# Kernel optimization log

Hardware: AMD Instinct MI355X
Metric: run time of the kernel (lower is better)

Reference implementation:

```python
import jax, jax.numpy as jnp
import numpy as np

# Dimensions (see shape_source)
IN_VEC = 131072          # input_vector_size
NUM_CAPS = 512           # num_capsules (output capsules)
CAP_SIZE = 256           # capsule_size
RF_SIZE = 64             # receptive_field_size
RF_PER_CAP = CAP_SIZE // RF_SIZE        # 4
IN_CAPS = IN_VEC // CAP_SIZE            # 512 input_eff_capsules
CONN_P = 0.1             # connection_probability


def setup_inputs() -> dict:
    key = jax.random.key(0)
    kx, kc, kw = jax.random.split(key, 3)
    x = jax.random.normal(kx, (IN_VEC,), dtype=jnp.float32)
    # Sparse ScRRAMBLe routing tensor: mostly zeros, gated by connection probability.
    # Shape (input_eff_capsules, rf_per_cap_in, num_capsules, rf_per_cap_out) per einsum 'ijkl,ijm->klm'.
    Ci = (jax.random.uniform(kc, (IN_CAPS, RF_PER_CAP, NUM_CAPS, RF_PER_CAP)) < CONN_P).astype(jnp.float32)
    # glorot_normal over last two axes: fan_in = fan_out = RF_SIZE -> std = sqrt(2/(64+64)) = 0.125
    glorot_std = float(np.sqrt(2.0 / (RF_SIZE + RF_SIZE)))
    Wi = glorot_std * jax.random.normal(kw, (NUM_CAPS, RF_PER_CAP, RF_PER_CAP, RF_SIZE, RF_SIZE), dtype=jnp.float32)
    return {"x": x, "Ci": Ci, "Wi": Wi}


def reference(x, Ci, Wi):
    # x: (IN_VEC,) -> (input_eff_capsules, rf_per_cap, rf_size)
    x_reshaped = x.reshape(IN_CAPS, RF_PER_CAP, RF_SIZE)
    # Route input receptive fields to output capsule slots:
    # x_routed: (num_capsules, rf_per_cap, rf_size)
    x_routed = jnp.einsum('ijkl,ijm->klm', Ci, x_reshaped)
    # Per-capsule small batched transform:
    # y: (num_capsules, rf_per_cap, rf_size)
    y = jnp.einsum('ijklm,ikm->ijl', Wi, x_routed)
    return y
```

## Files before the change

### kernel.cpp

```cpp
#include <hip/hip_runtime.h>


typedef float f4 __attribute__((ext_vector_type(4)));

#define NCH 8

__global__ __launch_bounds__(256) void route_kernel(
    const float* __restrict__ x,
    const float* __restrict__ Ci,
    float* __restrict__ xr_part)
{
    const int iq  = blockIdx.x;
    const int c   = blockIdx.y;
    const int t   = threadIdx.x;
    const int il  = t >> 6;
    const int g   = (t >> 4) & 3;
    const int mq4 = t & 15;
    const int i   = (iq << 2) + il;

    const f4* __restrict__ Ci4 = (const f4*)Ci;
    const f4* __restrict__ x4  = (const f4*)x;

    __shared__ f4 part[1024];

    f4 a0 = {0.f,0.f,0.f,0.f};
    f4 a1 = {0.f,0.f,0.f,0.f};
    f4 a2 = {0.f,0.f,0.f,0.f};
    f4 a3 = {0.f,0.f,0.f,0.f};

    const int ijpc = 2048 / NCH;
    const int sub  = ijpc >> 2;
    const int base = c * ijpc + g * sub;
    #pragma unroll 4
    for (int it = 0; it < sub; ++it) {
        const int ij = base + it;
        const f4 c4 = Ci4[ij * 512 + i];
        const f4 xv = x4[(ij << 4) + mq4];
        a0 += c4.x * xv;
        a1 += c4.y * xv;
        a2 += c4.z * xv;
        a3 += c4.w * xv;
    }

    const int pb = ((g << 2) + il) << 2;
    part[(pb + 0) * 16 + mq4] = a0;
    part[(pb + 1) * 16 + mq4] = a1;
    part[(pb + 2) * 16 + mq4] = a2;
    part[(pb + 3) * 16 + mq4] = a3;
    __syncthreads();

    const int il2 = t >> 6;
    const int r   = (t >> 4) & 3;
    const int mm  = t & 15;
    f4 s = {0.f,0.f,0.f,0.f};
    #pragma unroll
    for (int gg = 0; gg < 4; ++gg)
        s += part[(((gg << 2) + il2) * 4 + r) * 16 + mm];

    f4* __restrict__ xp4 = (f4*)xr_part;
    xp4[(c * 512 + (iq << 2) + il2) * 64 + r * 16 + mm] = s;
}

__global__ __launch_bounds__(256, 4) void transform_kernel(
    const float* __restrict__ Wi,
    const float* __restrict__ xr_part,
    float* __restrict__ y)
{
    const int b    = blockIdx.x;
    const int i    = b >> 2;
    const int t    = threadIdx.x;
    const int lane = t & 63;
    const int w    = t >> 6;
    const int lq   = lane >> 4;
    const int m16  = lane & 15;

    const f4* __restrict__ W4 = (const f4*)Wi;
    const int wbase = b * 4096;
    const int lw    = w << 4;

    f4 wv[16];
    #pragma unroll
    for (int c2 = 0; c2 < 4; ++c2) {
        const int l = lw + (c2 << 2) + lq;
        #pragma unroll
        for (int k = 0; k < 4; ++k)
            wv[(c2 << 2) + k] =
                __builtin_nontemporal_load(&W4[wbase + (k << 10) + l * 16 + m16]);
    }

    const f4* __restrict__ xp4 = (const f4*)xr_part;
    f4 xr0 = {0.f,0.f,0.f,0.f};
    f4 xr1 = {0.f,0.f,0.f,0.f};
    f4 xr2 = {0.f,0.f,0.f,0.f};
    f4 xr3 = {0.f,0.f,0.f,0.f};
    #pragma unroll
    for (int c = 0; c < NCH; ++c) {
        const int base = (c * 512 + i) * 64;
        xr0 += xp4[base + 0 * 16 + m16];
        xr1 += xp4[base + 1 * 16 + m16];
        xr2 += xp4[base + 2 * 16 + m16];
        xr3 += xp4[base + 3 * 16 + m16];
    }

    #pragma unroll
    for (int c2 = 0; c2 < 4; ++c2) {
        const int l = lw + (c2 << 2) + lq;
        f4 s = wv[(c2 << 2) + 0] * xr0
             + wv[(c2 << 2) + 1] * xr1
             + wv[(c2 << 2) + 2] * xr2
             + wv[(c2 << 2) + 3] * xr3;
        float p = s.x + s.y + s.z + s.w;
        p += __shfl_xor(p, 1);
        p += __shfl_xor(p, 2);
        p += __shfl_xor(p, 4);
        p += __shfl_xor(p, 8);
        if (m16 == 0) y[b * 64 + l] = p;
    }
}

extern "C" void kernel_launch(void* const* d_in, const int* in_sizes, int n_in,
                              void* d_out, int out_size, void* d_ws, size_t ws_size,
                              hipStream_t stream) {
    const float* x  = (const float*)d_in[0];
    const float* Ci = (const float*)d_in[1];
    const float* Wi = (const float*)d_in[2];
    float* y  = (float*)d_out;
    float* xr = (float*)d_ws;

    route_kernel<<<dim3(128, NCH), 256, 0, stream>>>(x, Ci, xr);
    transform_kernel<<<2048, 256, 0, stream>>>(Wi, xr, y);
}
```

Baseline: 221.2 us.

## Fuse routing and transform into one per-capsule kernel with prefetched weights

Merges the routing and transform kernels into one kernel launched with one block per output capsule. Each block computes its routed input vector in registers and shared memory, which removes the workspace round-trip and the second launch. The first weight group is loaded before the routing loop and later groups are double-buffered, so weight traffic overlaps routing and compute. In exchange, every block now reads the whole input vector and walks Ci with a broadcast, strided access pattern over a long serial loop. The grid also shrinks to 512 blocks, which may leave the GPU latency-bound.

```diff
diff --git a/kernel.cpp b/kernel.cpp
--- a/kernel.cpp
+++ b/kernel.cpp
@@ -3,119 +3,87 @@
 
 typedef float f4 __attribute__((ext_vector_type(4)));
 
-#define NCH 8
-
-__global__ __launch_bounds__(256) void route_kernel(
+__global__ __launch_bounds__(256, 2) void fused_caps_kernel(
     const float* __restrict__ x,
     const float* __restrict__ Ci,
-    float* __restrict__ xr_part)
-{
-    const int iq  = blockIdx.x;
-    const int c   = blockIdx.y;
-    const int t   = threadIdx.x;
-    const int il  = t >> 6;
-    const int g   = (t >> 4) & 3;
-    const int mq4 = t & 15;
-    const int i   = (iq << 2) + il;
-
-    const f4* __restrict__ Ci4 = (const f4*)Ci;
-    const f4* __restrict__ x4  = (const f4*)x;
-
-    __shared__ f4 part[1024];
-
-    f4 a0 = {0.f,0.f,0.f,0.f};
-    f4 a1 = {0.f,0.f,0.f,0.f};
-    f4 a2 = {0.f,0.f,0.f,0.f};
-    f4 a3 = {0.f,0.f,0.f,0.f};
-
-    const int ijpc = 2048 / NCH;
-    const int sub  = ijpc >> 2;
-    const int base = c * ijpc + g * sub;
-    #pragma unroll 4
-    for (int it = 0; it < sub; ++it) {
-        const int ij = base + it;
-        const f4 c4 = Ci4[ij * 512 + i];
-        const f4 xv = x4[(ij << 4) + mq4];
-        a0 += c4.x * xv;
-        a1 += c4.y * xv;
-        a2 += c4.z * xv;
-        a3 += c4.w * xv;
-    }
-
-    const int pb = ((g << 2) + il) << 2;
-    part[(pb + 0) * 16 + mq4] = a0;
-    part[(pb + 1) * 16 + mq4] = a1;
-    part[(pb + 2) * 16 + mq4] = a2;
-    part[(pb + 3) * 16 + mq4] = a3;
-    __syncthreads();
-
-    const int il2 = t >> 6;
-    const int r   = (t >> 4) & 3;
-    const int mm  = t & 15;
-    f4 s = {0.f,0.f,0.f,0.f};
-    #pragma unroll
-    for (int gg = 0; gg < 4; ++gg)
-        s += part[(((gg << 2) + il2) * 4 + r) * 16 + mm];
-
-    f4* __restrict__ xp4 = (f4*)xr_part;
-    xp4[(c * 512 + (iq << 2) + il2) * 64 + r * 16 + mm] = s;
-}
-
-__global__ __launch_bounds__(256, 4) void transform_kernel(
     const float* __restrict__ Wi,
-    const float* __restrict__ xr_part,
     float* __restrict__ y)
 {
-    const int b    = blockIdx.x;
-    const int i    = b >> 2;
+    const int c    = blockIdx.x;
     const int t    = threadIdx.x;
+    const int w    = t >> 6;
     const int lane = t & 63;
-    const int w    = t >> 6;
     const int lq   = lane >> 4;
     const int m16  = lane & 15;
 
-    const f4* __restrict__ W4 = (const f4*)Wi;
-    const int wbase = b * 4096;
-    const int lw    = w << 4;
+    const f4* __restrict__ Ci4 = (const f4*)Ci;
+    const f4* __restrict__ W4  = (const f4*)Wi;
 
-    f4 wv[16];
-    #pragma unroll
-    for (int c2 = 0; c2 < 4; ++c2) {
-        const int l = lw + (c2 << 2) + lq;
-        #pragma unroll
-        for (int k = 0; k < 4; ++k)
-            wv[(c2 << 2) + k] =
-                __builtin_nontemporal_load(&W4[wbase + (k << 10) + l * 16 + m16]);
+    __shared__ float part[4 * 4 * 64];
+
+    const int wbase = ((c << 2) + w) << 12;
+
+    f4 wvA[16], wvB[16];
+
+#define PREFETCH(dst, g4)                                                   \
+    _Pragma("unroll")                                                       \
+    for (int c2 = 0; c2 < 4; ++c2) {                                        \
+        const int l = ((g4) << 4) + (c2 << 2) + lq;                         \
+        _Pragma("unroll")                                                   \
+        for (int k = 0; k < 4; ++k)                                         \
+            dst[(c2 << 2) + k] = W4[wbase + (k << 10) + l * 16 + m16];      \
     }
 
-    const f4* __restrict__ xp4 = (const f4*)xr_part;
-    f4 xr0 = {0.f,0.f,0.f,0.f};
-    f4 xr1 = {0.f,0.f,0.f,0.f};
-    f4 xr2 = {0.f,0.f,0.f,0.f};
-    f4 xr3 = {0.f,0.f,0.f,0.f};
-    #pragma unroll
-    for (int c = 0; c < NCH; ++c) {
-        const int base = (c * 512 + i) * 64;
-        xr0 += xp4[base + 0 * 16 + m16];
-        xr1 += xp4[base + 1 * 16 + m16];
-        xr2 += xp4[base + 2 * 16 + m16];
-        xr3 += xp4[base + 3 * 16 + m16];
+#define COMPUTE(src, g4)                                                    \
+    _Pragma("unroll")                                                       \
+    for (int c2 = 0; c2 < 4; ++c2) {                                        \
+        f4 s = src[(c2 << 2) + 0] * xr0 + src[(c2 << 2) + 1] * xr1          \
+             + src[(c2 << 2) + 2] * xr2 + src[(c2 << 2) + 3] * xr3;         \
+        float p = s.x + s.y + s.z + s.w;                                    \
+        p += __shfl_xor(p, 1);                                              \
+        p += __shfl_xor(p, 2);                                              \
+        p += __shfl_xor(p, 4);                                              \
+        p += __shfl_xor(p, 8);                                              \
+        if (m16 == 0)                                                       \
+            y[(((c << 2) + w) << 6) + ((g4) << 4) + (c2 << 2) + lq] = p;    \
     }
 
-    #pragma unroll
-    for (int c2 = 0; c2 < 4; ++c2) {
-        const int l = lw + (c2 << 2) + lq;
-        f4 s = wv[(c2 << 2) + 0] * xr0
-             + wv[(c2 << 2) + 1] * xr1
-             + wv[(c2 << 2) + 2] * xr2
-             + wv[(c2 << 2) + 3] * xr3;
-        float p = s.x + s.y + s.z + s.w;
-        p += __shfl_xor(p, 1);
-        p += __shfl_xor(p, 2);
-        p += __shfl_xor(p, 4);
-        p += __shfl_xor(p, 8);
-        if (m16 == 0) y[b * 64 + l] = p;
+    PREFETCH(wvA, 0)
+
+    f4 acc = {0.f, 0.f, 0.f, 0.f};
+    {
+        const int ij0 = w << 9;
+        const float* __restrict__ xp = x + lane;
+        #pragma unroll 8
+        for (int it = 0; it < 512; ++it) {
+            const int ij   = ij0 + it;
+            const f4 cv    = Ci4[ij * 512 + c];
+            const float xv = xp[ij << 6];
+            acc += cv * xv;
+        }
     }
+    part[(w << 8) +   0 + lane] = acc.x;
+    part[(w << 8) +  64 + lane] = acc.y;
+    part[(w << 8) + 128 + lane] = acc.z;
+    part[(w << 8) + 192 + lane] = acc.w;
+    __syncthreads();
+
+    const f4* partf4 = (const f4*)part;
+    f4 xr0 = partf4[  0 + m16] + partf4[ 64 + m16] + partf4[128 + m16] + partf4[192 + m16];
+    f4 xr1 = partf4[ 16 + m16] + partf4[ 80 + m16] + partf4[144 + m16] + partf4[208 + m16];
+    f4 xr2 = partf4[ 32 + m16] + partf4[ 96 + m16] + partf4[160 + m16] + partf4[224 + m16];
+    f4 xr3 = partf4[ 48 + m16] + partf4[112 + m16] + partf4[176 + m16] + partf4[240 + m16];
+
+    PREFETCH(wvB, 1)
+    COMPUTE(wvA, 0)
+    PREFETCH(wvA, 2)
+    COMPUTE(wvB, 1)
+    PREFETCH(wvB, 3)
+    COMPUTE(wvA, 2)
+    COMPUTE(wvB, 3)
+
+#undef PREFETCH
+#undef COMPUTE
 }
 
 extern "C" void kernel_launch(void* const* d_in, const int* in_sizes, int n_in,
@@ -124,9 +92,7 @@
     const float* x  = (const float*)d_in[0];
     const float* Ci = (const float*)d_in[1];
     const float* Wi = (const float*)d_in[2];
-    float* y  = (float*)d_out;
-    float* xr = (float*)d_ws;
+    float* y = (float*)d_out;
 
-    route_kernel<<<dim3(128, NCH), 256, 0, stream>>>(x, Ci, xr);
-    transform_kernel<<<2048, 256, 0, stream>>>(Wi, xr, y);
+    fused_caps_kernel<<<512, 256, 0, stream>>>(x, Ci, Wi, y);
 }
```

Result: slower. 241.6 us (+9.3%).

## Stage Ci and x tiles in shared memory for routing, split reduction into 16 chunks

Applied to the files above, without the earlier changes.

The routing kernel now has each block load a 128-row slab of Ci (16 output capsules wide) and the matching x slab into LDS, then compute full partial sums per thread without the cross-group LDS reduction. The reduction dimension is split into 16 chunks instead of 8, with 32x16 blocks, so the transform kernel sums 16 partials. The aim is to improve coalescing of the Ci reads and reuse of x across threads, at the cost of 64 KB of LDS per block, lower occupancy and more partial-sum traffic.

```diff
diff --git a/kernel.cpp b/kernel.cpp
--- a/kernel.cpp
+++ b/kernel.cpp
@@ -3,62 +3,55 @@
 
 typedef float f4 __attribute__((ext_vector_type(4)));
 
-#define NCH 8
+#define NCH 16
 
-__global__ __launch_bounds__(256) void route_kernel(
+__global__ __launch_bounds__(256, 2) void route_kernel(
     const float* __restrict__ x,
     const float* __restrict__ Ci,
     float* __restrict__ xr_part)
 {
-    const int iq  = blockIdx.x;
-    const int c   = blockIdx.y;
-    const int t   = threadIdx.x;
-    const int il  = t >> 6;
-    const int g   = (t >> 4) & 3;
-    const int mq4 = t & 15;
-    const int i   = (iq << 2) + il;
+    const int cg = blockIdx.x;
+    const int ch = blockIdx.y;
+    const int t  = threadIdx.x;
 
     const f4* __restrict__ Ci4 = (const f4*)Ci;
     const f4* __restrict__ x4  = (const f4*)x;
 
-    __shared__ f4 part[1024];
+    __shared__ f4 ci_s[2048];
+    __shared__ f4 x_s[2048];
 
+    #pragma unroll
+    for (int u = 0; u < 8; ++u) {
+        const int e   = (u << 8) + t;
+        const int ijl = e >> 4;
+        const int cc  = e & 15;
+        ci_s[e] = Ci4[((ch << 7) + ijl) * 512 + (cg << 4) + cc];
+        x_s[e]  = x4[(ch << 11) + e];
+    }
+    __syncthreads();
+
+    const int cc = t >> 4;
+    const int mq = t & 15;
     f4 a0 = {0.f,0.f,0.f,0.f};
     f4 a1 = {0.f,0.f,0.f,0.f};
     f4 a2 = {0.f,0.f,0.f,0.f};
     f4 a3 = {0.f,0.f,0.f,0.f};
-
-    const int ijpc = 2048 / NCH;
-    const int sub  = ijpc >> 2;
-    const int base = c * ijpc + g * sub;
     #pragma unroll 4
-    for (int it = 0; it < sub; ++it) {
-        const int ij = base + it;
-        const f4 c4 = Ci4[ij * 512 + i];
-        const f4 xv = x4[(ij << 4) + mq4];
-        a0 += c4.x * xv;
-        a1 += c4.y * xv;
-        a2 += c4.z * xv;
-        a3 += c4.w * xv;
+    for (int ij = 0; ij < 128; ++ij) {
+        const f4 civ = ci_s[(ij << 4) + cc];
+        const f4 xv  = x_s[(ij << 4) + mq];
+        a0 += civ.x * xv;
+        a1 += civ.y * xv;
+        a2 += civ.z * xv;
+        a3 += civ.w * xv;
     }
 
-    const int pb = ((g << 2) + il) << 2;
-    part[(pb + 0) * 16 + mq4] = a0;
-    part[(pb + 1) * 16 + mq4] = a1;
-    part[(pb + 2) * 16 + mq4] = a2;
-    part[(pb + 3) * 16 + mq4] = a3;
-    __syncthreads();
-
-    const int il2 = t >> 6;
-    const int r   = (t >> 4) & 3;
-    const int mm  = t & 15;
-    f4 s = {0.f,0.f,0.f,0.f};
-    #pragma unroll
-    for (int gg = 0; gg < 4; ++gg)
-        s += part[(((gg << 2) + il2) * 4 + r) * 16 + mm];
-
     f4* __restrict__ xp4 = (f4*)xr_part;
-    xp4[(c * 512 + (iq << 2) + il2) * 64 + r * 16 + mm] = s;
+    const int base = ((ch << 9) + (cg << 4) + cc) << 2;
+    xp4[(base + 0) * 16 + mq] = a0;
+    xp4[(base + 1) * 16 + mq] = a1;
+    xp4[(base + 2) * 16 + mq] = a2;
+    xp4[(base + 3) * 16 + mq] = a3;
 }
 
 __global__ __launch_bounds__(256, 4) void transform_kernel(
@@ -75,7 +68,7 @@
     const int m16  = lane & 15;
 
     const f4* __restrict__ W4 = (const f4*)Wi;
-    const int wbase = b * 4096;
+    const int wbase = b << 12;
     const int lw    = w << 4;
 
     f4 wv[16];
@@ -93,13 +86,13 @@
     f4 xr1 = {0.f,0.f,0.f,0.f};
     f4 xr2 = {0.f,0.f,0.f,0.f};
     f4 xr3 = {0.f,0.f,0.f,0.f};
-    #pragma unroll
-    for (int c = 0; c < NCH; ++c) {
-        const int base = (c * 512 + i) * 64;
-        xr0 += xp4[base + 0 * 16 + m16];
-        xr1 += xp4[base + 1 * 16 + m16];
-        xr2 += xp4[base + 2 * 16 + m16];
-        xr3 += xp4[base + 3 * 16 + m16];
+    #pragma unroll 4
+    for (int ch = 0; ch < NCH; ++ch) {
+        const int base = ((ch << 9) + i) << 2;
+        xr0 += xp4[(base + 0) * 16 + m16];
+        xr1 += xp4[(base + 1) * 16 + m16];
+        xr2 += xp4[(base + 2) * 16 + m16];
+        xr3 += xp4[(base + 3) * 16 + m16];
     }
 
     #pragma unroll
@@ -114,7 +107,7 @@
         p += __shfl_xor(p, 2);
         p += __shfl_xor(p, 4);
         p += __shfl_xor(p, 8);
-        if (m16 == 0) y[b * 64 + l] = p;
+        if (m16 == 0) y[(b << 6) + l] = p;
     }
 }
 
@@ -127,6 +120,6 @@
     float* y  = (float*)d_out;
     float* xr = (float*)d_ws;
 
-    route_kernel<<<dim3(128, NCH), 256, 0, stream>>>(x, Ci, xr);
+    route_kernel<<<dim3(32, NCH), 256, 0, stream>>>(x, Ci, xr);
     transform_kernel<<<2048, 256, 0, stream>>>(Wi, xr, y);
 }
```

Result: slower. 236.8 us (+7.1%).
